# Performance work log

Hardware: AMD Instinct MI355X
Metric: run time of the kernel (lower is better)

The kernel has to match this reference:

```python
import jax, jax.numpy as jnp
import numpy as np

N_NODES = 100000
N_EDGES = 1600000
N_FEAT = 128
HIDDEN = 128
N_CLASSES = 40
MAX_DEPTH = 4
INIT_TEMP = 1.0  # temperature (non-trainable)
N_AGGR = 3       # ['mean', 'max', 'self']


def setup_inputs() -> dict:
    key = jax.random.key(0)
    ks = jax.random.split(key, 16)
    s = 1.0 / np.sqrt(HIDDEN)
    inp = {
        'x': jax.random.normal(ks[0], (N_NODES, N_FEAT), dtype=jnp.float32),
        'edge_index': jax.random.randint(ks[1], (2, N_EDGES), 0, N_NODES, dtype=jnp.int32),
        'W_pre': jax.random.normal(ks[2], (N_FEAT, HIDDEN), dtype=jnp.float32) / np.sqrt(N_FEAT),
        'b_pre': jnp.zeros((HIDDEN,), dtype=jnp.float32),
        'W_depth': jax.random.normal(ks[3], (HIDDEN, 2), dtype=jnp.float32) * s,
        'b_depth': jnp.zeros((2,), dtype=jnp.float32),
        'W_aggr': jax.random.normal(ks[4], (HIDDEN, N_AGGR), dtype=jnp.float32) * s,
        'b_aggr': jnp.zeros((N_AGGR,), dtype=jnp.float32),
        'W_conv': jax.random.normal(ks[5], (MAX_DEPTH, HIDDEN, HIDDEN), dtype=jnp.float32) * s,
        'b_conv': jnp.zeros((MAX_DEPTH, HIDDEN), dtype=jnp.float32),
        'W_post': jax.random.normal(ks[6], (HIDDEN, N_CLASSES), dtype=jnp.float32) * s,
        'b_post': jnp.zeros((N_CLASSES,), dtype=jnp.float32),
    }
    return inp


def _mix_aggr_conv(x, src, dst, deg, W, b, aggr_w):
    # MixAggrConvLayer: transform then per-node convex mix of {mean, max, self}
    h = x @ W + b                                   # [N, H]
    msg = h[src]                                    # [E, H] gather
    mean_a = jax.ops.segment_sum(msg, dst, num_segments=N_NODES) / deg[:, None]
    max_a = jax.ops.segment_max(msg, dst, num_segments=N_NODES)
    max_a = jnp.where(jnp.isfinite(max_a), max_a, 0.0)  # isolated nodes -> 0
    return aggr_w[:, 0:1] * mean_a + aggr_w[:, 1:2] * max_a + aggr_w[:, 2:3] * h


def reference(x, edge_index, W_pre, b_pre, W_depth, b_depth, W_aggr, b_aggr,
              W_conv, b_conv, W_post, b_post):
    src, dst = edge_index[0], edge_index[1]
    deg = jnp.maximum(
        jax.ops.segment_sum(jnp.ones((src.shape[0],), jnp.float32), dst,
                            num_segments=N_NODES), 1.0)

    # pre_mp + (Dropout eval = identity) + ReLU
    h = jax.nn.relu(x @ W_pre + b_pre)              # [N, H]

    continue_pr = jnp.ones((N_NODES,), jnp.float32)
    selected = jnp.zeros((N_NODES, HIDDEN), jnp.float32)
    for i in range(MAX_DEPTH):
        hd = jax.lax.stop_gradient(h)               # controllers see detached x
        stop_prob = jax.nn.softmax((hd @ W_depth + b_depth) / INIT_TEMP, axis=-1)
        aggr_prob = jax.nn.softmax((hd @ W_aggr + b_aggr) / INIT_TEMP, axis=-1)
        h = _mix_aggr_conv(h, src, dst, deg, W_conv[i], b_conv[i], aggr_prob)
        h = jax.nn.relu(h)                          # dropout (eval) + relu
        selected = selected + (continue_pr * stop_prob[:, 1])[:, None] * h
        continue_pr = continue_pr * stop_prob[:, 0]

    logits = selected @ W_post + b_post             # [N, C]
    return jax.nn.log_softmax(logits, axis=1)
```

## Files before the change

### kernel.cpp

```cpp
#include <hip/hip_runtime.h>
#include <math.h>

#define HIDDEN 128
#define NCLS 40
#define BMAX 1024

typedef __attribute__((ext_vector_type(8))) short short8;
typedef __attribute__((ext_vector_type(4))) float f32x4;

__device__ __forceinline__ unsigned short f2bf(float f) {
    unsigned u = __float_as_uint(f);
    unsigned r = u + 0x7FFFu + ((u >> 16) & 1u);
    return (unsigned short)(r >> 16);
}
__device__ __forceinline__ float bf_lo(unsigned u) { return __uint_as_float(u << 16); }
__device__ __forceinline__ float bf_hi(unsigned u) { return __uint_as_float(u & 0xFFFF0000u); }

__global__ void k_wt(const float* __restrict__ W, unsigned short* __restrict__ Wt, int total) {
    int i = blockIdx.x * 256 + threadIdx.x;
    if (i < total) {
        int n = (i >> 7) & 127, k = i & 127;
        Wt[i] = f2bf(W[k * 128 + n]);
    }
}

__global__ void k_wtc(const float* __restrict__ Wc, const float* __restrict__ Wd,
                      const float* __restrict__ Wa, unsigned short* __restrict__ WT,
                      int total) {
    int i = blockIdx.x * 256 + threadIdx.x;
    if (i < total) {
        int d = i / 18432;
        int rem = i % 18432;
        int n = rem >> 7, k = rem & 127;
        float v = 0.f;
        if (n < 128)      v = Wc[d * 16384 + k * 128 + n];
        else if (n < 130) v = Wd[k * 2 + (n - 128)];
        else if (n < 133) v = Wa[k * 3 + (n - 130)];
        WT[i] = f2bf(v);
    }
}


__launch_bounds__(256)
__global__ void k_bcount(const int* __restrict__ ei, int E, int* __restrict__ bucket_cnt) {
    __shared__ int hist[BMAX];
    const int tid = threadIdx.x;
    for (int i = tid; i < BMAX; i += 256) hist[i] = 0;
    __syncthreads();
    const int e0 = blockIdx.x * 4096;
    #pragma unroll
    for (int i = 0; i < 16; i++) {
        int e = e0 + i * 256 + tid;
        if (e < E) atomicAdd(&hist[ei[E + e] >> 8], 1);
    }
    __syncthreads();
    for (int i = tid; i < BMAX; i += 256) {
        int v = hist[i];
        if (v > 0) atomicAdd(&bucket_cnt[i], v);
    }
}

__global__ void k_bscan(const int* __restrict__ bucket_cnt, int nb,
                        int* __restrict__ bucket_base, int* __restrict__ bucket_cursor) {
    __shared__ int sd[256];
    const int tid = threadIdx.x;
    int v[4];
    int sum = 0;
    #pragma unroll
    for (int j = 0; j < 4; j++) {
        int b = tid * 4 + j;
        v[j] = (b < nb) ? bucket_cnt[b] : 0;
        sum += v[j];
    }
    sd[tid] = sum;
    __syncthreads();
    #pragma unroll
    for (int off = 1; off < 256; off <<= 1) {
        int t = (tid >= off) ? sd[tid - off] : 0;
        __syncthreads();
        sd[tid] += t;
        __syncthreads();
    }
    int base = sd[tid] - sum;
    #pragma unroll
    for (int j = 0; j < 4; j++) {
        int b = tid * 4 + j;
        if (b < nb) {
            bucket_base[b] = base;
            bucket_cursor[b] = base;
            base += v[j];
        }
    }
}

__launch_bounds__(256)
__global__ void k_bin(const int* __restrict__ ei, int E,
                      int* __restrict__ bucket_cursor, unsigned* __restrict__ binned) {
    __shared__ int hist[BMAX];
    __shared__ int rankc[BMAX];
    __shared__ int lbase[BMAX];
    const int tid = threadIdx.x;
    const int e0 = blockIdx.x * 4096;
    for (int i = tid; i < BMAX; i += 256) { hist[i] = 0; rankc[i] = 0; }
    __syncthreads();
    int bkt[16];
    unsigned pk[16];
    #pragma unroll
    for (int i = 0; i < 16; i++) {
        int e = e0 + i * 256 + tid;
        if (e < E) {
            int s = ei[e];
            int d = ei[E + e];
            bkt[i] = d >> 8;
            pk[i] = ((unsigned)(d & 255) << 24) | (unsigned)s;
            atomicAdd(&hist[bkt[i]], 1);
        } else bkt[i] = -1;
    }
    __syncthreads();
    for (int i = tid; i < BMAX; i += 256)
        if (hist[i] > 0) lbase[i] = atomicAdd(&bucket_cursor[i], hist[i]);
    __syncthreads();
    #pragma unroll
    for (int i = 0; i < 16; i++) {
        if (bkt[i] >= 0) {
            int r = atomicAdd(&rankc[bkt[i]], 1);
            binned[lbase[bkt[i]] + r] = pk[i];
        }
    }
}

__launch_bounds__(256)
__global__ void k_scatter(const unsigned* __restrict__ binned,
                          const int* __restrict__ bucket_base,
                          const int* __restrict__ bucket_cnt,
                          int* __restrict__ row_start, int* __restrict__ deg_i,
                          float* __restrict__ degf,
                          int* __restrict__ csr_off, int N) {
    __shared__ int hist[256];
    __shared__ int rs[256];
    __shared__ int cur[256];
    const int tid = threadIdx.x;
    hist[tid] = 0;
    __syncthreads();
    const int base = bucket_base[blockIdx.x];
    const int cnt = bucket_cnt[blockIdx.x];
    for (int i = tid; i < cnt; i += 256)
        atomicAdd(&hist[binned[base + i] >> 24], 1);
    __syncthreads();
    int v = hist[tid];
    rs[tid] = v;
    __syncthreads();
    #pragma unroll
    for (int off = 1; off < 256; off <<= 1) {
        int t = (tid >= off) ? rs[tid - off] : 0;
        __syncthreads();
        rs[tid] += t;
        __syncthreads();
    }
    int gstart = base + rs[tid] - v;
    int n = (blockIdx.x << 8) + tid;
    if (n < N) {
        row_start[n] = gstart;
        deg_i[n] = v;
        degf[n] = fmaxf((float)v, 1.0f);
    }
    __syncthreads();
    rs[tid] = gstart;
    cur[tid] = 0;
    __syncthreads();
    for (int i = tid; i < cnt; i += 256) {
        unsigned p = binned[base + i];
        int dl = (int)(p >> 24);
        int r = atomicAdd(&cur[dl], 1);
        csr_off[rs[dl] + r] = (int)((p & 0xFFFFFFu) << 8);
    }
}


template <bool AF32, bool CTRL>
__launch_bounds__(256)
__global__ void k_gemm_mfma(const void* __restrict__ Ain,
                            const unsigned short* __restrict__ Wt,
                            const float* __restrict__ bias,
                            unsigned short* __restrict__ Cb,
                            float* __restrict__ ctrl,
                            int M, int do_relu) {
    __shared__ unsigned short Ws[144 * 132];
    const int tid = threadIdx.x;
    const int lane = tid & 63;
    const int wv = tid >> 6;
    const int row_blk = blockIdx.x * 128;
    const int rows0 = (wv >> 1) * 64;
    const int cols0 = (wv & 1) * 64;
    const int l15 = lane & 15;
    const int q = lane >> 4;
    const int RWS = CTRL ? 144 : 128;

    for (int c = tid; c < RWS * 16; c += 256) {
        int r = c >> 4, ch = c & 15;
        *(uint4*)&Ws[r * 132 + ch * 8] = *(const uint4*)(Wt + (size_t)r * HIDDEN + ch * 8);
    }
    __syncthreads();

    f32x4 acc[4][4] = {};
    f32x4 acc5[4] = {};
    for (int k0 = 0; k0 < 128; k0 += 32) {
        short8 af[4];
        #pragma unroll
        for (int mi = 0; mi < 4; mi++) {
            int ar = row_blk + rows0 + mi * 16 + l15;
            if (AF32) {
                const float* A = (const float*)Ain;
                float4 v0 = make_float4(0.f, 0.f, 0.f, 0.f);
                float4 v1 = make_float4(0.f, 0.f, 0.f, 0.f);
                if (ar < M) {
                    v0 = *(const float4*)(A + (size_t)ar * HIDDEN + k0 + q * 8);
                    v1 = *(const float4*)(A + (size_t)ar * HIDDEN + k0 + q * 8 + 4);
                }
                short8 t;
                t[0] = (short)f2bf(v0.x); t[1] = (short)f2bf(v0.y);
                t[2] = (short)f2bf(v0.z); t[3] = (short)f2bf(v0.w);
                t[4] = (short)f2bf(v1.x); t[5] = (short)f2bf(v1.y);
                t[6] = (short)f2bf(v1.z); t[7] = (short)f2bf(v1.w);
                af[mi] = t;
            } else {
                const unsigned short* A = (const unsigned short*)Ain;
                short8 t = {};
                if (ar < M) t = *(const short8*)(A + (size_t)ar * HIDDEN + k0 + q * 8);
                af[mi] = t;
            }
        }
        #pragma unroll
        for (int ni = 0; ni < 4; ni++) {
            short8 bw = *(const short8*)&Ws[(cols0 + ni * 16 + l15) * 132 + k0 + q * 8];
            #pragma unroll
            for (int mi = 0; mi < 4; mi++)
                acc[mi][ni] = __builtin_amdgcn_mfma_f32_16x16x32_bf16(
                    bw, af[mi], acc[mi][ni], 0, 0, 0);
        }
        if (CTRL && (wv & 1) == 0) {
            short8 bc = *(const short8*)&Ws[(128 + l15) * 132 + k0 + q * 8];
            #pragma unroll
            for (int mi = 0; mi < 4; mi++)
                acc5[mi] = __builtin_amdgcn_mfma_f32_16x16x32_bf16(
                    bc, af[mi], acc5[mi], 0, 0, 0);
        }
    }
    #pragma unroll
    for (int mi = 0; mi < 4; mi++) {
        int node = row_blk + rows0 + mi * 16 + l15;
        if (node < M) {
            #pragma unroll
            for (int ni = 0; ni < 4; ni++) {
                int fb = cols0 + ni * 16 + q * 4;
                float4 bv = *(const float4*)&bias[fb];
                float o0 = acc[mi][ni][0] + bv.x;
                float o1 = acc[mi][ni][1] + bv.y;
                float o2 = acc[mi][ni][2] + bv.z;
                float o3 = acc[mi][ni][3] + bv.w;
                if (do_relu) {
                    o0 = fmaxf(o0, 0.f); o1 = fmaxf(o1, 0.f);
                    o2 = fmaxf(o2, 0.f); o3 = fmaxf(o3, 0.f);
                }
                ushort4 ov;
                ov.x = f2bf(o0); ov.y = f2bf(o1); ov.z = f2bf(o2); ov.w = f2bf(o3);
                *(ushort4*)(Cb + (size_t)node * HIDDEN + fb) = ov;
            }
            if (CTRL && (wv & 1) == 0) {
                if (q == 0) {
                    *(float4*)(ctrl + (size_t)node * 8) =
                        make_float4(acc5[mi][0], acc5[mi][1], acc5[mi][2], acc5[mi][3]);
                } else if (q == 1) {
                    ctrl[(size_t)node * 8 + 4] = acc5[mi][0];
                }
            }
        }
    }
}


__launch_bounds__(256)
__global__ void k_depth(const unsigned short* __restrict__ ht,
                        unsigned short* __restrict__ h_out,
                        float* __restrict__ cp, float* __restrict__ wsel,
                        const float* __restrict__ ctrl,
                        const float* __restrict__ degf, const int* __restrict__ deg_i,
                        const int* __restrict__ row_start, const int* __restrict__ csr_off,
                        const float* __restrict__ bd, const float* __restrict__ ba,
                        int N, int first) {
    const int lane = threadIdx.x & 63;
    const int wave = threadIdx.x >> 6;
    const int node = blockIdx.x * 4 + wave;
    if (node >= N) return;
    const int nodeu = __builtin_amdgcn_readfirstlane(node);
    const int half = lane >> 5;
    const int fb = (lane & 31) * 4;
    const int fob = fb * 2;
    const char* htb = (const char*)ht;

    float4 c4 = *(const float4*)(ctrl + (size_t)nodeu * 8);
    float cl4 = ctrl[(size_t)nodeu * 8 + 4];
    float d0 = c4.x + bd[0], d1 = c4.y + bd[1];
    float a0 = c4.z + ba[0], a1 = c4.w + ba[1], a2 = cl4 + ba[2];
    float m2 = fmaxf(d0, d1);
    float e0 = __expf(d0 - m2), e1 = __expf(d1 - m2);
    float inv2 = 1.f / (e0 + e1);
    float sp0 = e0 * inv2, sp1 = e1 * inv2;
    float m3 = fmaxf(fmaxf(a0, a1), a2);
    float f0 = __expf(a0 - m3), f1 = __expf(a1 - m3), f2 = __expf(a2 - m3);
    float inv3 = 1.f / (f0 + f1 + f2);
    float ap0 = f0 * inv3, ap1 = f1 * inv3, ap2 = f2 * inv3;

    const int cnt = deg_i[nodeu];
    const int start = row_start[nodeu];
    const float invd = 1.0f / degf[nodeu];

    float s0 = 0.f, s1 = 0.f, s2 = 0.f, s3 = 0.f;
    float x0m = -3.4e38f, x1m = -3.4e38f, x2m = -3.4e38f, x3m = -3.4e38f;

    for (int eb = 0; eb < cnt; eb += 64) {
        int idx = eb + lane;
        int soff = (idx < cnt) ? csr_off[start + idx] : 0;
        int lim = min(64, cnt - eb);
        int lim2 = lim & ~1;
        int j = 0;
        #define GPAIR(JJ)                                                     \
        {                                                                     \
            int o = __shfl(soff, (JJ) + half);                                \
            uint2 u = *(const uint2*)(htb + (unsigned)(o + fob));             \
            float px0 = bf_lo(u.x), px1 = bf_hi(u.x);                         \
            float px2 = bf_lo(u.y), px3 = bf_hi(u.y);                         \
            s0 += px0; s1 += px1; s2 += px2; s3 += px3;                       \
            x0m = fmaxf(x0m, px0); x1m = fmaxf(x1m, px1);                     \
            x2m = fmaxf(x2m, px2); x3m = fmaxf(x3m, px3);                     \
        }
        for (; j + 8 <= lim2; j += 8) { GPAIR(j) GPAIR(j + 2) GPAIR(j + 4) GPAIR(j + 6) }
        for (; j < lim2; j += 2) GPAIR(j)
        #undef GPAIR
        if (lim & 1) {
            int o = __shfl(soff, lim - 1);
            if (half == 0) {
                uint2 u = *(const uint2*)(htb + (unsigned)(o + fob));
                float px0 = bf_lo(u.x), px1 = bf_hi(u.x);
                float px2 = bf_lo(u.y), px3 = bf_hi(u.y);
                s0 += px0; s1 += px1; s2 += px2; s3 += px3;
                x0m = fmaxf(x0m, px0); x1m = fmaxf(x1m, px1);
                x2m = fmaxf(x2m, px2); x3m = fmaxf(x3m, px3);
            }
        }
    }
    s0 += __shfl_xor(s0, 32); s1 += __shfl_xor(s1, 32);
    s2 += __shfl_xor(s2, 32); s3 += __shfl_xor(s3, 32);
    x0m = fmaxf(x0m, __shfl_xor(x0m, 32)); x1m = fmaxf(x1m, __shfl_xor(x1m, 32));
    x2m = fmaxf(x2m, __shfl_xor(x2m, 32)); x3m = fmaxf(x3m, __shfl_xor(x3m, 32));

    if (cnt == 0) { x0m = 0.f; x1m = 0.f; x2m = 0.f; x3m = 0.f; }

    if (half == 0) {
        uint2 su = *(const uint2*)(htb + (unsigned)(nodeu * 256 + fob));
        float h0 = ap0 * (s0 * invd) + ap1 * x0m + ap2 * bf_lo(su.x);
        float h1 = ap0 * (s1 * invd) + ap1 * x1m + ap2 * bf_hi(su.x);
        float h2 = ap0 * (s2 * invd) + ap1 * x2m + ap2 * bf_lo(su.y);
        float h3 = ap0 * (s3 * invd) + ap1 * x3m + ap2 * bf_hi(su.y);
        h0 = fmaxf(h0, 0.f); h1 = fmaxf(h1, 0.f);
        h2 = fmaxf(h2, 0.f); h3 = fmaxf(h3, 0.f);
        ushort4 ho;
        ho.x = f2bf(h0); ho.y = f2bf(h1); ho.z = f2bf(h2); ho.w = f2bf(h3);
        *(ushort4*)(h_out + (size_t)nodeu * HIDDEN + fb) = ho;
    }
    if (lane == 0) {
        float cpv = first ? 1.0f : cp[nodeu];
        wsel[nodeu] = cpv * sp1;
        cp[nodeu] = cpv * sp0;
    }
}


__launch_bounds__(256)
__global__ void k_post(const unsigned short* __restrict__ h_all, size_t hstride,
                       const float* __restrict__ wsel, int N,
                       const float* __restrict__ Wp, const float* __restrict__ bp,
                       float* __restrict__ out) {
    __shared__ float Ss[32][132];
    __shared__ float Wt[NCLS][132];
    __shared__ float bs[NCLS];
    const int tid = threadIdx.x;
    const int n0 = blockIdx.x * 32;

    for (int i = tid; i < (HIDDEN * NCLS) / 4; i += 256) {
        float4 v = *(const float4*)&Wp[i * 4];
        int f = i * 4;
        int k = f / NCLS, c = f % NCLS;
        float e[4] = {v.x, v.y, v.z, v.w};
        #pragma unroll
        for (int j = 0; j < 4; j++) {
            int cc = c + j, kk = k;
            if (cc >= NCLS) { cc -= NCLS; kk++; }
            Wt[cc][kk] = e[j];
        }
    }
    if (tid < NCLS) bs[tid] = bp[tid];

    const int node_l = tid >> 3;
    const int kc = (tid & 7) * 16;
    const int ng = n0 + node_l;
    float sel[16];
    #pragma unroll
    for (int i = 0; i < 16; i++) sel[i] = 0.f;
    if (ng < N) {
        #pragma unroll
        for (int d = 0; d < 4; d++) {
            float w = wsel[(size_t)d * N + ng];
            const unsigned short* hrow = h_all + (size_t)(d + 1) * hstride + (size_t)ng * HIDDEN;
            #pragma unroll
            for (int u = 0; u < 2; u++) {
                uint4 p = *(const uint4*)(hrow + kc + u * 8);
                unsigned vs[4] = {p.x, p.y, p.z, p.w};
                #pragma unroll
                for (int j = 0; j < 4; j++) {
                    sel[u * 8 + j * 2 + 0] += w * bf_lo(vs[j]);
                    sel[u * 8 + j * 2 + 1] += w * bf_hi(vs[j]);
                }
            }
        }
    }
    #pragma unroll
    for (int u = 0; u < 4; u++)
        *(float4*)&Ss[node_l][kc + u * 4] =
            make_float4(sel[u * 4], sel[u * 4 + 1], sel[u * 4 + 2], sel[u * 4 + 3]);
    __syncthreads();

    const int c0 = (tid & 7) * 5;
    float z[5];
    #pragma unroll
    for (int i = 0; i < 5; i++) z[i] = bs[c0 + i];
    for (int k = 0; k < HIDDEN; k += 4) {
        float4 s4 = *(const float4*)&Ss[node_l][k];
        #pragma unroll
        for (int i = 0; i < 5; i++) {
            float4 w4 = *(const float4*)&Wt[c0 + i][k];
            z[i] += s4.x * w4.x + s4.y * w4.y + s4.z * w4.z + s4.w * w4.w;
        }
    }
    float m = z[0];
    #pragma unroll
    for (int i = 1; i < 5; i++) m = fmaxf(m, z[i]);
    #pragma unroll
    for (int off = 1; off < 8; off <<= 1) m = fmaxf(m, __shfl_xor(m, off));
    float s = 0.f;
    #pragma unroll
    for (int i = 0; i < 5; i++) s += expf(z[i] - m);
    #pragma unroll
    for (int off = 1; off < 8; off <<= 1) s += __shfl_xor(s, off);
    float lg = m + logf(s);
    if (ng < N) {
        #pragma unroll
        for (int i = 0; i < 5; i++)
            out[(size_t)ng * NCLS + c0 + i] = z[i] - lg;
    }
}


extern "C" void kernel_launch(void* const* d_in, const int* in_sizes, int n_in,
                              void* d_out, int out_size, void* d_ws, size_t ws_size,
                              hipStream_t stream) {
    const float* x      = (const float*)d_in[0];
    const int*   ei     = (const int*)d_in[1];
    const float* W_pre  = (const float*)d_in[2];
    const float* b_pre  = (const float*)d_in[3];
    const float* W_dep  = (const float*)d_in[4];
    const float* b_dep  = (const float*)d_in[5];
    const float* W_aggr = (const float*)d_in[6];
    const float* b_aggr = (const float*)d_in[7];
    const float* W_conv = (const float*)d_in[8];
    const float* b_conv = (const float*)d_in[9];
    const float* W_post = (const float*)d_in[10];
    const float* b_post = (const float*)d_in[11];

    const int N = in_sizes[0] / HIDDEN;
    const int E = in_sizes[1] / 2;
    const int nbuckets = (N + 255) >> 8;

    char* ws = (char*)d_ws;
    size_t off = 0;
    auto alloc = [&](size_t bytes) -> void* {
        void* p = ws + off;
        off += (bytes + 255) & ~(size_t)255;
        return p;
    };
    const size_t hstride = (size_t)N * HIDDEN;
    unsigned short* h_all  = (unsigned short*)alloc(5 * hstride * 2);
    unsigned short* ht     = (unsigned short*)alloc(hstride * 2);
    float* cp       = (float*)alloc((size_t)N * 4);
    float* wsel     = (float*)alloc((size_t)4 * N * 4);
    float* degf     = (float*)alloc((size_t)N * 4);
    float* ctrl     = (float*)alloc((size_t)N * 8 * 4);
    unsigned short* WpreT = (unsigned short*)alloc(128 * 128 * 2);
    unsigned short* WT    = (unsigned short*)alloc(4 * 144 * 128 * 2);
    int*   deg_i    = (int*)alloc((size_t)N * 4);
    int*   row_start= (int*)alloc((size_t)N * 4);
    int*   bucket_cnt    = (int*)alloc(BMAX * 4);
    int*   bucket_base   = (int*)alloc(BMAX * 4);
    int*   bucket_cursor = (int*)alloc(BMAX * 4);
    int*   csr_off  = (int*)alloc((size_t)E * 4);
    unsigned* binned = (unsigned*)alloc((size_t)E * 4);

    hipMemsetAsync(bucket_cnt, 0, BMAX * 4, stream);

    int ebb = (E + 4095) / 4096;
    k_bcount<<<ebb, 256, 0, stream>>>(ei, E, bucket_cnt);
    k_bscan<<<1, 256, 0, stream>>>(bucket_cnt, nbuckets, bucket_base, bucket_cursor);
    k_bin<<<ebb, 256, 0, stream>>>(ei, E, bucket_cursor, binned);
    k_scatter<<<nbuckets, 256, 0, stream>>>(binned, bucket_base, bucket_cnt,
                                            row_start, deg_i, degf, csr_off, N);

    k_wt<<<(16384 + 255) / 256, 256, 0, stream>>>(W_pre, WpreT, 16384);
    k_wtc<<<(4 * 18432 + 255) / 256, 256, 0, stream>>>(W_conv, W_dep, W_aggr, WT, 4 * 18432);

    int gblk = (N + 127) / 128;
    k_gemm_mfma<true, false><<<gblk, 256, 0, stream>>>(x, WpreT, b_pre, h_all,
                                                       nullptr, N, 1);

    int nb4 = (N + 3) / 4;
    for (int d = 0; d < 4; d++) {
        unsigned short* h_d  = h_all + (size_t)d * hstride;
        unsigned short* h_n  = h_all + (size_t)(d + 1) * hstride;
        k_gemm_mfma<false, true><<<gblk, 256, 0, stream>>>(h_d, WT + (size_t)d * 18432,
                                                           b_conv + (size_t)d * HIDDEN,
                                                           ht, ctrl, N, 0);
        k_depth<<<nb4, 256, 0, stream>>>(ht, h_n, cp, wsel + (size_t)d * N, ctrl,
                                         degf, deg_i, row_start, csr_off,
                                         b_dep, b_aggr, N, d == 0 ? 1 : 0);
    }
    k_post<<<(N + 31) / 32, 256, 0, stream>>>(h_all, hstride, wsel, N,
                                              W_post, b_post, (float*)d_out);
}
```

Baseline: 594.7 us.

## Merge weight-prep kernels, retile GEMM waves to full width, deepen gather unroll

Combines the two weight transpose/convert kernels into one launch to save launch overhead. The MFMA GEMM changes from a 2x2 wave tiling (64 rows x 64 cols per wave) to each wave covering 32 rows x all 128 columns. A-fragments are now loaded once per row instead of duplicated across column halves, and every wave computes its own controller outputs. The edge-gather loop in the depth kernel is unrolled to 16 edges per iteration for more memory-level parallelism, at the cost of more register pressure.

```diff
diff --git a/kernel.cpp b/kernel.cpp
--- a/kernel.cpp
+++ b/kernel.cpp
@@ -16,27 +16,23 @@
 __device__ __forceinline__ float bf_lo(unsigned u) { return __uint_as_float(u << 16); }
 __device__ __forceinline__ float bf_hi(unsigned u) { return __uint_as_float(u & 0xFFFF0000u); }
 
-__global__ void k_wt(const float* __restrict__ W, unsigned short* __restrict__ Wt, int total) {
+__global__ void k_wprep(const float* __restrict__ Wp, const float* __restrict__ Wc,
+                        const float* __restrict__ Wd, const float* __restrict__ Wa,
+                        unsigned short* __restrict__ WpreT, unsigned short* __restrict__ WT) {
     int i = blockIdx.x * 256 + threadIdx.x;
-    if (i < total) {
-        int n = (i >> 7) & 127, k = i & 127;
-        Wt[i] = f2bf(W[k * 128 + n]);
-    }
-}
-
-__global__ void k_wtc(const float* __restrict__ Wc, const float* __restrict__ Wd,
-                      const float* __restrict__ Wa, unsigned short* __restrict__ WT,
-                      int total) {
-    int i = blockIdx.x * 256 + threadIdx.x;
-    if (i < total) {
-        int d = i / 18432;
-        int rem = i % 18432;
+    if (i < 16384) {
+        int n = i >> 7, k = i & 127;
+        WpreT[i] = f2bf(Wp[k * 128 + n]);
+    } else if (i < 16384 + 4 * 18432) {
+        int j = i - 16384;
+        int d = j / 18432;
+        int rem = j % 18432;
         int n = rem >> 7, k = rem & 127;
         float v = 0.f;
         if (n < 128)      v = Wc[d * 16384 + k * 128 + n];
         else if (n < 130) v = Wd[k * 2 + (n - 128)];
         else if (n < 133) v = Wa[k * 3 + (n - 130)];
-        WT[i] = f2bf(v);
+        WT[j] = f2bf(v);
     }
 }
 
@@ -190,8 +186,7 @@
     const int lane = tid & 63;
     const int wv = tid >> 6;
     const int row_blk = blockIdx.x * 128;
-    const int rows0 = (wv >> 1) * 64;
-    const int cols0 = (wv & 1) * 64;
+    const int rows0 = wv * 32;
     const int l15 = lane & 15;
     const int q = lane >> 4;
     const int RWS = CTRL ? 144 : 128;
@@ -202,12 +197,12 @@
     }
     __syncthreads();
 
-    f32x4 acc[4][4] = {};
-    f32x4 acc5[4] = {};
+    f32x4 acc[2][8] = {};
+    f32x4 acc5[2] = {};
     for (int k0 = 0; k0 < 128; k0 += 32) {
-        short8 af[4];
+        short8 af[2];
         #pragma unroll
-        for (int mi = 0; mi < 4; mi++) {
+        for (int mi = 0; mi < 2; mi++) {
             int ar = row_blk + rows0 + mi * 16 + l15;
             if (AF32) {
                 const float* A = (const float*)Ain;
@@ -231,28 +226,28 @@
             }
         }
         #pragma unroll
-        for (int ni = 0; ni < 4; ni++) {
-            short8 bw = *(const short8*)&Ws[(cols0 + ni * 16 + l15) * 132 + k0 + q * 8];
+        for (int ni = 0; ni < 8; ni++) {
+            short8 bw = *(const short8*)&Ws[(ni * 16 + l15) * 132 + k0 + q * 8];
             #pragma unroll
-            for (int mi = 0; mi < 4; mi++)
+            for (int mi = 0; mi < 2; mi++)
                 acc[mi][ni] = __builtin_amdgcn_mfma_f32_16x16x32_bf16(
                     bw, af[mi], acc[mi][ni], 0, 0, 0);
         }
-        if (CTRL && (wv & 1) == 0) {
+        if (CTRL) {
             short8 bc = *(const short8*)&Ws[(128 + l15) * 132 + k0 + q * 8];
             #pragma unroll
-            for (int mi = 0; mi < 4; mi++)
+            for (int mi = 0; mi < 2; mi++)
                 acc5[mi] = __builtin_amdgcn_mfma_f32_16x16x32_bf16(
                     bc, af[mi], acc5[mi], 0, 0, 0);
         }
     }
     #pragma unroll
-    for (int mi = 0; mi < 4; mi++) {
+    for (int mi = 0; mi < 2; mi++) {
         int node = row_blk + rows0 + mi * 16 + l15;
         if (node < M) {
             #pragma unroll
-            for (int ni = 0; ni < 4; ni++) {
-                int fb = cols0 + ni * 16 + q * 4;
+            for (int ni = 0; ni < 8; ni++) {
+                int fb = ni * 16 + q * 4;
                 float4 bv = *(const float4*)&bias[fb];
                 float o0 = acc[mi][ni][0] + bv.x;
                 float o1 = acc[mi][ni][1] + bv.y;
@@ -266,7 +261,7 @@
                 ov.x = f2bf(o0); ov.y = f2bf(o1); ov.z = f2bf(o2); ov.w = f2bf(o3);
                 *(ushort4*)(Cb + (size_t)node * HIDDEN + fb) = ov;
             }
-            if (CTRL && (wv & 1) == 0) {
+            if (CTRL) {
                 if (q == 0) {
                     *(float4*)(ctrl + (size_t)node * 8) =
                         make_float4(acc5[mi][0], acc5[mi][1], acc5[mi][2], acc5[mi][3]);
@@ -334,7 +329,11 @@
             x0m = fmaxf(x0m, px0); x1m = fmaxf(x1m, px1);                     \
             x2m = fmaxf(x2m, px2); x3m = fmaxf(x3m, px3);                     \
         }
-        for (; j + 8 <= lim2; j += 8) { GPAIR(j) GPAIR(j + 2) GPAIR(j + 4) GPAIR(j + 6) }
+        for (; j + 16 <= lim2; j += 16) {
+            GPAIR(j) GPAIR(j + 2) GPAIR(j + 4) GPAIR(j + 6)
+            GPAIR(j + 8) GPAIR(j + 10) GPAIR(j + 12) GPAIR(j + 14)
+        }
+        for (; j + 4 <= lim2; j += 4) { GPAIR(j) GPAIR(j + 2) }
         for (; j < lim2; j += 2) GPAIR(j)
         #undef GPAIR
         if (lim & 1) {
@@ -514,8 +513,9 @@
     k_scatter<<<nbuckets, 256, 0, stream>>>(binned, bucket_base, bucket_cnt,
                                             row_start, deg_i, degf, csr_off, N);
 
-    k_wt<<<(16384 + 255) / 256, 256, 0, stream>>>(W_pre, WpreT, 16384);
-    k_wtc<<<(4 * 18432 + 255) / 256, 256, 0, stream>>>(W_conv, W_dep, W_aggr, WT, 4 * 18432);
+    int wtot = 16384 + 4 * 18432;
+    k_wprep<<<(wtot + 255) / 256, 256, 0, stream>>>(W_pre, W_conv, W_dep, W_aggr,
+                                                    WpreT, WT);
 
     int gblk = (N + 127) / 128;
     k_gemm_mfma<true, false><<<gblk, 256, 0, stream>>>(x, WpreT, b_pre, h_all,
```

Result: no change. 583.4 us (-1.9%).
